# Performance work log

Measured on AMD Instinct MI355X. Metric: run time of the kernel, lower is better.

The kernel has to match this reference:

```python
import jax, jax.numpy as jnp
import numpy as np

B, S, IN, H = 64, 512, 256, 256
NH, E = 8, 5
DH = H // NH


def _ln(x, g, b, eps=1e-5):
    m = jnp.mean(x, -1, keepdims=True)
    v = jnp.mean((x - m) ** 2, -1, keepdims=True)
    return (x - m) / jnp.sqrt(v + eps) * g + b


def setup_inputs() -> dict:
    key = jax.random.key(0)
    ks = jax.random.split(key, 32)
    def p(i, shape, scale=0.05):
        return jax.random.normal(ks[i], shape, dtype=jnp.float32) * scale
    return {
        "x": jax.random.normal(ks[0], (B, S, IN), dtype=jnp.float32),
        "lengths": jax.random.randint(ks[1], (B,), 1, S + 1),
        "fe_w": p(2, (H, IN)), "fe_b": p(3, (H,)),
        "fe_ln_g": jnp.ones((H,), jnp.float32), "fe_ln_b": jnp.zeros((H,), jnp.float32),
        "w_ih": p(4, (4 * H, H)), "w_hh": p(5, (4 * H, H)),
        "b_ih": p(6, (4 * H,)), "b_hh": p(7, (4 * H,)),
        "attn_w": p(8, (3 * H, H)), "attn_b": p(9, (3 * H,)),
        "attn_ow": p(10, (H, H)), "attn_ob": p(11, (H,)),
        "ln1_g": jnp.ones((H,), jnp.float32), "ln1_b": jnp.zeros((H,), jnp.float32),
        "router_w": p(12, (H, E)),
        "e_w1": p(13, (E, H, H)), "e_b1": p(14, (E, H)),
        "e_w2": p(15, (E, H, H)), "e_b2": p(16, (E, H)),
        "ln2_g": jnp.ones((H,), jnp.float32), "ln2_b": jnp.zeros((H,), jnp.float32),
        "cl_w1": p(17, (H, H)), "cl_b1": p(18, (H,)),
        "cl_ln_g": jnp.ones((H,), jnp.float32), "cl_ln_b": jnp.zeros((H,), jnp.float32),
        "cl_w2": p(19, (1, H)), "cl_b2": p(20, (1,)),
    }


def _forward(x, lengths, fe_w, fe_b, fe_ln_g, fe_ln_b, w_ih, w_hh, b_ih, b_hh,
             attn_w, attn_b, attn_ow, attn_ob, ln1_g, ln1_b, router_w,
             e_w1, e_b1, e_w2, e_b2, ln2_g, ln2_b,
             cl_w1, cl_b1, cl_ln_g, cl_ln_b, cl_w2, cl_b2):
    # feature extractor: Linear -> LayerNorm -> ReLU (dropout off at eval)
    h0 = jax.nn.relu(_ln(x @ fe_w.T + fe_b, fe_ln_g, fe_ln_b))  # [B,S,H]
    # single-layer LSTM over padded sequence (causal => matches packed outputs at t < len)
    def step(carry, xt):
        h, c = carry
        z = xt @ w_ih.T + b_ih + h @ w_hh.T + b_hh  # PyTorch gate order i,f,g,o
        i, f, g, o = jnp.split(z, 4, axis=-1)
        c = jax.nn.sigmoid(f) * c + jax.nn.sigmoid(i) * jnp.tanh(g)
        h = jax.nn.sigmoid(o) * jnp.tanh(c)
        return (h, c), h
    init = (jnp.zeros((B, H), x.dtype), jnp.zeros((B, H), x.dtype))
    _, outs = jax.lax.scan(step, init, jnp.swapaxes(h0, 0, 1))
    lstm_out = jnp.swapaxes(outs, 0, 1)  # [B,S,H]
    valid = jnp.arange(S)[None, :] < lengths[:, None]  # [B,S]
    lstm_out = lstm_out * valid[..., None]  # pad_packed_sequence zeros
    # multi-head self-attention with key padding mask
    qkv = lstm_out @ attn_w.T + attn_b
    q, k, v = jnp.split(qkv, 3, axis=-1)
    q = q.reshape(B, S, NH, DH)
    k = k.reshape(B, S, NH, DH)
    v = v.reshape(B, S, NH, DH)
    scores = jnp.einsum("bqhd,bkhd->bhqk", q, k) / jnp.sqrt(jnp.float32(DH))
    scores = jnp.where(valid[:, None, None, :], scores, jnp.float32(-1e9))
    attn = jax.nn.softmax(scores, axis=-1)
    ao = jnp.einsum("bhqk,bkhd->bqhd", attn, v).reshape(B, S, H)
    ao = ao @ attn_ow.T + attn_ob
    src = _ln(lstm_out + ao, ln1_g, ln1_b)  # post-norm residual
    # Switch (top-1) MoE FFN
    probs = jax.nn.softmax(src @ router_w, axis=-1)  # [B,S,E]
    idx = jnp.argmax(probs, axis=-1)                 # [B,S]
    gate = jnp.take_along_axis(probs, idx[..., None], axis=-1)  # [B,S,1]
    eh = jax.nn.relu(jnp.einsum("bsd,edh->bseh", src, e_w1) + e_b1)
    ey = jnp.einsum("bseh,ehd->bsed", eh, e_w2) + e_b2          # [B,S,E,H]
    ysel = jnp.take_along_axis(ey, idx[:, :, None, None], axis=2)[:, :, 0, :]
    out = _ln(src + gate * ysel, ln2_g, ln2_b)
    # masked mean pool
    out = out * valid[..., None]
    pooled = out.sum(axis=1) / lengths[:, None].astype(jnp.float32)
    # classifier head
    hcl = jax.nn.relu(_ln(pooled @ cl_w1.T + cl_b1, cl_ln_g, cl_ln_b))
    return hcl @ cl_w2.T + cl_b2  # [B,1]


def reference(x, lengths, fe_w, fe_b, fe_ln_g, fe_ln_b, w_ih, w_hh, b_ih, b_hh,
              attn_w, attn_b, attn_ow, attn_ob, ln1_g, ln1_b, router_w,
              e_w1, e_b1, e_w2, e_b2, ln2_g, ln2_b,
              cl_w1, cl_b1, cl_ln_g, cl_ln_b, cl_w2, cl_b2):
    return _forward(x, lengths, fe_w, fe_b, fe_ln_g, fe_ln_b, w_ih, w_hh, b_ih, b_hh,
                    attn_w, attn_b, attn_ow, attn_ob, ln1_g, ln1_b, router_w,
                    e_w1, e_b1, e_w2, e_b2, ln2_g, ln2_b,
                    cl_w1, cl_b1, cl_ln_g, cl_ln_b, cl_w2, cl_b2)
```

## Files before the change

kernel.cpp:

```cpp
#include <hip/hip_runtime.h>
#include <cstdio>
#include <math.h>

#define BB 64
#define SS 512
#define HH 256
#define G4 1024
#define TT (BB*SS)

typedef _Float16 h2 __attribute__((ext_vector_type(2)));
typedef _Float16 h8 __attribute__((ext_vector_type(8)));
typedef float f4v __attribute__((ext_vector_type(4)));

__device__ __forceinline__ float sigf(float x){ return 1.0f/(1.0f+expf(-x)); }

__global__ void prep_kernel(const float* __restrict__ b_ih, const float* __restrict__ b_hh,
                            float* __restrict__ bcomb, float* __restrict__ hglob,
                            unsigned* __restrict__ cnt){
    int i = blockIdx.x*blockDim.x + threadIdx.x;
    if (i < G4) bcomb[i] = b_ih[i] + b_hh[i];
    if (i < 8)  cnt[i] = 0u;
    hglob[i] = 0.f;
}

__global__ __launch_bounds__(256) void gemm_mfma(
    const float* __restrict__ A, const float* __restrict__ Bw,
    const float* __restrict__ bias, float* __restrict__ C,
    int N, const int* __restrict__ lengths)
{
    int m0 = blockIdx.y * 128, n0 = blockIdx.x * 128;
    if (lengths){ int b = m0 >> 9, t0 = m0 & 511; if (t0 >= lengths[b]) return; }
    __shared__ _Float16 Asd[128][40];
    __shared__ _Float16 Bsd[128][40];
    int tid = threadIdx.x;
    int wave = tid >> 6, lane = tid & 63;
    int wr = (wave >> 1) * 64, wc = (wave & 1) * 64;
    int fr = lane & 15, fk = (lane >> 4) * 8;
    int srow = tid >> 1, skh = (tid & 1) * 16;
    const float* gA = A  + (size_t)(m0 + srow)*256 + skh;
    const float* gB = Bw + (size_t)(n0 + srow)*256 + skh;
    f4v acc[4][4];
    #pragma unroll
    for (int i=0;i<4;i++)
        #pragma unroll
        for (int j=0;j<4;j++) acc[i][j] = (f4v){0.f,0.f,0.f,0.f};

    for (int kt = 0; kt < 8; ++kt){
        int k0 = kt*32;
        float4 a0 = *(const float4*)(gA + k0);
        float4 a1 = *(const float4*)(gA + k0 + 4);
        float4 a2 = *(const float4*)(gA + k0 + 8);
        float4 a3 = *(const float4*)(gA + k0 + 12);
        float4 b0 = *(const float4*)(gB + k0);
        float4 b1 = *(const float4*)(gB + k0 + 4);
        float4 b2 = *(const float4*)(gB + k0 + 8);
        float4 b3 = *(const float4*)(gB + k0 + 12);
        __syncthreads();
        {
            _Float16* da = &Asd[srow][skh];
            h2 t;
            t.x=(_Float16)a0.x; t.y=(_Float16)a0.y; *(h2*)(da+0)=t;
            t.x=(_Float16)a0.z; t.y=(_Float16)a0.w; *(h2*)(da+2)=t;
            t.x=(_Float16)a1.x; t.y=(_Float16)a1.y; *(h2*)(da+4)=t;
            t.x=(_Float16)a1.z; t.y=(_Float16)a1.w; *(h2*)(da+6)=t;
            t.x=(_Float16)a2.x; t.y=(_Float16)a2.y; *(h2*)(da+8)=t;
            t.x=(_Float16)a2.z; t.y=(_Float16)a2.w; *(h2*)(da+10)=t;
            t.x=(_Float16)a3.x; t.y=(_Float16)a3.y; *(h2*)(da+12)=t;
            t.x=(_Float16)a3.z; t.y=(_Float16)a3.w; *(h2*)(da+14)=t;
            _Float16* db = &Bsd[srow][skh];
            t.x=(_Float16)b0.x; t.y=(_Float16)b0.y; *(h2*)(db+0)=t;
            t.x=(_Float16)b0.z; t.y=(_Float16)b0.w; *(h2*)(db+2)=t;
            t.x=(_Float16)b1.x; t.y=(_Float16)b1.y; *(h2*)(db+4)=t;
            t.x=(_Float16)b1.z; t.y=(_Float16)b1.w; *(h2*)(db+6)=t;
            t.x=(_Float16)b2.x; t.y=(_Float16)b2.y; *(h2*)(db+8)=t;
            t.x=(_Float16)b2.z; t.y=(_Float16)b2.w; *(h2*)(db+10)=t;
            t.x=(_Float16)b3.x; t.y=(_Float16)b3.y; *(h2*)(db+12)=t;
            t.x=(_Float16)b3.z; t.y=(_Float16)b3.w; *(h2*)(db+14)=t;
        }
        __syncthreads();
        h8 af[4], bf[4];
        #pragma unroll
        for (int mt=0;mt<4;mt++) af[mt] = *(const h8*)&Asd[wr + mt*16 + fr][fk];
        #pragma unroll
        for (int nt=0;nt<4;nt++) bf[nt] = *(const h8*)&Bsd[wc + nt*16 + fr][fk];
        #pragma unroll
        for (int mt=0;mt<4;mt++)
            #pragma unroll
            for (int nt=0;nt<4;nt++)
                acc[mt][nt] = __builtin_amdgcn_mfma_f32_16x16x32_f16(af[mt], bf[nt], acc[mt][nt], 0,0,0);
    }
    int rbase = m0 + wr + (lane>>4)*4;
    #pragma unroll
    for (int nt=0;nt<4;nt++){
        int col = n0 + wc + nt*16 + fr;
        float bv = bias ? bias[col] : 0.f;
        #pragma unroll
        for (int mt=0;mt<4;mt++){
            int row = rbase + mt*16;
            #pragma unroll
            for (int j=0;j<4;j++)
                C[(size_t)(row+j)*N + col] = acc[mt][nt][j] + bv;
        }
    }
}

__global__ __launch_bounds__(256) void ln_act(
    float* __restrict__ X, const float* __restrict__ add,
    const float* __restrict__ gg, const float* __restrict__ bb,
    const int* __restrict__ lengths, int relu)
{
    int row = blockIdx.x;
    { int b = row >> 9, t = row & 511; if (t >= lengths[b]) return; }
    int tid = threadIdx.x;
    __shared__ float red[8];
    size_t idx = (size_t)row*HH + tid;
    float v = X[idx];
    if (add) v += add[idx];
    float s = v, q = v*v;
    #pragma unroll
    for (int m=32;m>=1;m>>=1){ s += __shfl_xor(s,m); q += __shfl_xor(q,m); }
    if ((tid&63)==0){ red[tid>>6]=s; red[4+(tid>>6)]=q; }
    __syncthreads();
    s = red[0]+red[1]+red[2]+red[3]; q = red[4]+red[5]+red[6]+red[7];
    float mean = s*(1.f/HH);
    float var  = q*(1.f/HH) - mean*mean;
    float rstd = rsqrtf(var + 1e-5f);
    float o = (v-mean)*rstd*gg[tid] + bb[tid];
    if (relu) o = fmaxf(o, 0.f);
    X[idx] = o;
}

__global__ __launch_bounds__(512) void lstm_kernel(
    const float* __restrict__ Zx, const float* __restrict__ whh,
    const int* __restrict__ lengths, float* __restrict__ hglob,
    float* __restrict__ out)
{
    int bid = blockIdx.x;
    int row = bid >> 1, p = bid & 1;
    int tid = threadIdx.x;
    __shared__ __align__(16) _Float16 hs_own[128];
    __shared__ __align__(16) _Float16 hs_rem[128];
    __shared__ float zfull[512];

    int q = tid >> 7, d = tid & 127;
    const float* wrow = whh + (size_t)(q*256 + p*128 + d)*256;
    const float* wown = wrow + p*128;
    const float* wrem = wrow + (1-p)*128;
    h2 wA[64], wB[64];
    #pragma unroll
    for (int c=0;c<32;c++){
        float4 w4 = *(const float4*)(wown + c*4);
        h2 a; a.x=(_Float16)w4.x; a.y=(_Float16)w4.y;
        h2 b; b.x=(_Float16)w4.z; b.y=(_Float16)w4.w;
        wA[2*c]=a; wA[2*c+1]=b;
    }
    #pragma unroll
    for (int c=0;c<32;c++){
        float4 w4 = *(const float4*)(wrem + c*4);
        h2 a; a.x=(_Float16)w4.x; a.y=(_Float16)w4.y;
        h2 b; b.x=(_Float16)w4.z; b.y=(_Float16)w4.w;
        wB[2*c]=a; wB[2*c+1]=b;
    }
    int Tg = lengths[row];
    float creg = 0.f;

    if (tid < 64) ((unsigned*)hs_own)[tid] = 0u;
    else if (tid < 128) ((unsigned*)hs_rem)[tid-64] = 0u;
    __syncthreads();

    float zx0=0.f, zx1=0.f, zx2=0.f, zx3=0.f;
    size_t zbase = (size_t)row*SS*G4 + (size_t)(p*128 + tid);
    if (tid < 128 && Tg > 0){
        zx0 = Zx[zbase      ];
        zx1 = Zx[zbase + 256];
        zx2 = Zx[zbase + 512];
        zx3 = Zx[zbase + 768];
    }

    unsigned long long* hgl64 = (unsigned long long*)hglob;
    union U16 { float4 f; h2 h[4]; };

    for (int s = 0; s < Tg; ++s){
        bool pollme = (tid < 64) && (s > 0);
        unsigned tagP = ((unsigned)s & 7u) ^ 5u;
        size_t paddr = ((size_t)((s&1)*64 + row)*2 + (1-p))*64 + tid;
        unsigned long long pv = 0;
        if (pollme) pv = __hip_atomic_load(&hgl64[paddr], __ATOMIC_RELAXED, __HIP_MEMORY_SCOPE_AGENT);

        float accA = 0.f, accB = 0.f;
        #pragma unroll
        for (int c=0;c<16;c++){
            U16 u; u.f = *(const float4*)&hs_own[c*8];
            accA = __builtin_amdgcn_fdot2(u.h[0], wA[c*4+0], accA, false);
            accB = __builtin_amdgcn_fdot2(u.h[1], wA[c*4+1], accB, false);
            accA = __builtin_amdgcn_fdot2(u.h[2], wA[c*4+2], accA, false);
            accB = __builtin_amdgcn_fdot2(u.h[3], wA[c*4+3], accB, false);
        }
        if (pollme){
            while ((((unsigned)pv & 7u) != tagP) || (((unsigned)(pv>>32) & 7u) != tagP))
                pv = __hip_atomic_load(&hgl64[paddr], __ATOMIC_RELAXED, __HIP_MEMORY_SCOPE_AGENT);
            h2 t; t.x = (_Float16)__uint_as_float((unsigned)pv);
            t.y = (_Float16)__uint_as_float((unsigned)(pv>>32));
            ((h2*)hs_rem)[tid] = t;
        }
        asm volatile("s_waitcnt lgkmcnt(0)" ::: "memory");
        __builtin_amdgcn_s_barrier();
        asm volatile("" ::: "memory");

        #pragma unroll
        for (int c=0;c<16;c++){
            U16 u; u.f = *(const float4*)&hs_rem[c*8];
            accA = __builtin_amdgcn_fdot2(u.h[0], wB[c*4+0], accA, false);
            accB = __builtin_amdgcn_fdot2(u.h[1], wB[c*4+1], accB, false);
            accA = __builtin_amdgcn_fdot2(u.h[2], wB[c*4+2], accA, false);
            accB = __builtin_amdgcn_fdot2(u.h[3], wB[c*4+3], accB, false);
        }
        zfull[tid] = accA + accB;
        asm volatile("s_waitcnt lgkmcnt(0)" ::: "memory");
        __builtin_amdgcn_s_barrier();
        asm volatile("" ::: "memory");

        if (tid < 128){
            float z0 = zfull[tid      ] + zx0;
            float z1 = zfull[128 + tid] + zx1;
            float z2 = zfull[256 + tid] + zx2;
            float z3 = zfull[384 + tid] + zx3;
            if (s+1 < Tg){
                size_t zb = zbase + (size_t)(s+1)*G4;
                zx0 = Zx[zb      ];
                zx1 = Zx[zb + 256];
                zx2 = Zx[zb + 512];
                zx3 = Zx[zb + 768];
            }
            creg = sigf(z1)*creg + sigf(z0)*tanhf(z2);
            float hvv = sigf(z3)*tanhf(creg);
            int buf2 = (s+1) & 1;
            unsigned tag2 = (((unsigned)(s+1)) & 7u) ^ 5u;
            unsigned hb = (__float_as_uint(hvv) & ~7u) | tag2;
            float hm = __uint_as_float(hb);
            __hip_atomic_store(&hglob[((size_t)(buf2*64 + row)*2 + p)*128 + tid],
                               hm, __ATOMIC_RELAXED, __HIP_MEMORY_SCOPE_AGENT);
            out[((size_t)row*SS + s)*HH + p*128 + tid] = hvv;
            hs_own[tid] = (_Float16)hm;
        }
        asm volatile("s_waitcnt lgkmcnt(0)" ::: "memory");
        __builtin_amdgcn_s_barrier();
        asm volatile("" ::: "memory");
    }
}

__global__ __launch_bounds__(256) void attn_kernel(
    const float* __restrict__ qkv, const int* __restrict__ lengths, float* __restrict__ ctx)
{
    int bh = blockIdx.x; int b = bh >> 3, h = bh & 7;
    int len = lengths[b];
    int tid = threadIdx.x;
    __shared__ float Ks[512][32];
    __shared__ float Vs[512][32];
    for (int i = tid; i < len*32; i += 256){
        int s = i >> 5, d = i & 31;
        size_t base = ((size_t)b*512 + s)*768 + h*32 + d;
        Ks[s][d] = qkv[base + 256];
        Vs[s][d] = qkv[base + 512];
    }
    __syncthreads();
    const float rs = 0.1767766952966369f;
    for (int q0 = 0; q0 < 512; q0 += 256){
        int q = q0 + tid;
        if (q >= len) continue;
        float qr[32];
        size_t qb = ((size_t)b*512 + q)*768 + h*32;
        #pragma unroll
        for (int d=0; d<32; d+=4){
            float4 t4 = *(const float4*)&qkv[qb+d];
            qr[d]=t4.x; qr[d+1]=t4.y; qr[d+2]=t4.z; qr[d+3]=t4.w;
        }
        float m = -3.4e38f, l = 0.f, acc[32];
        #pragma unroll
        for (int d=0;d<32;d++) acc[d]=0.f;
        for (int k=0;k<len;k++){
            float sc = 0.f;
            #pragma unroll
            for (int d=0;d<32;d+=4){
                float4 kv = *(const float4*)&Ks[k][d];
                sc += qr[d]*kv.x + qr[d+1]*kv.y + qr[d+2]*kv.z + qr[d+3]*kv.w;
            }
            sc *= rs;
            float nm = fmaxf(m, sc);
            float f  = expf(m - nm);
            float pc = expf(sc - nm);
            l = l*f + pc;
            #pragma unroll
            for (int d=0;d<32;d+=4){
                float4 vv = *(const float4*)&Vs[k][d];
                acc[d]   = acc[d]*f   + pc*vv.x;
                acc[d+1] = acc[d+1]*f + pc*vv.y;
                acc[d+2] = acc[d+2]*f + pc*vv.z;
                acc[d+3] = acc[d+3]*f + pc*vv.w;
            }
            m = nm;
        }
        float inv = 1.f/l;
        size_t cb = ((size_t)b*512 + q)*256 + h*32;
        #pragma unroll
        for (int d=0;d<32;d+=4){
            float4 o; o.x=acc[d]*inv; o.y=acc[d+1]*inv; o.z=acc[d+2]*inv; o.w=acc[d+3]*inv;
            *(float4*)&ctx[cb+d] = o;
        }
    }
}

__global__ __launch_bounds__(256) void route_kernel(
    const float* __restrict__ src, const float* __restrict__ rw,
    const int* __restrict__ lengths, unsigned* __restrict__ cnt,
    int* __restrict__ bucket, float* __restrict__ gates)
{
    int wv = threadIdx.x >> 6, lane = threadIdx.x & 63;
    int tok = blockIdx.x*4 + wv;
    int b = tok >> 9, t = tok & 511;
    if (t >= lengths[b]) return;
    float4 xv = *(const float4*)&src[(size_t)tok*256 + lane*4];
    float l0,l1,l2,l3,l4;
    {
        const float* r0 = &rw[(lane*4)*5];
        l0 = xv.x*r0[0] + xv.y*r0[5] + xv.z*r0[10] + xv.w*r0[15];
        l1 = xv.x*r0[1] + xv.y*r0[6] + xv.z*r0[11] + xv.w*r0[16];
        l2 = xv.x*r0[2] + xv.y*r0[7] + xv.z*r0[12] + xv.w*r0[17];
        l3 = xv.x*r0[3] + xv.y*r0[8] + xv.z*r0[13] + xv.w*r0[18];
        l4 = xv.x*r0[4] + xv.y*r0[9] + xv.z*r0[14] + xv.w*r0[19];
    }
    #pragma unroll
    for (int m=32;m>=1;m>>=1){
        l0 += __shfl_xor(l0,m); l1 += __shfl_xor(l1,m); l2 += __shfl_xor(l2,m);
        l3 += __shfl_xor(l3,m); l4 += __shfl_xor(l4,m);
    }
    if (lane == 0){
        float mx = l0; int ix = 0;
        if (l1 > mx){ mx=l1; ix=1; }
        if (l2 > mx){ mx=l2; ix=2; }
        if (l3 > mx){ mx=l3; ix=3; }
        if (l4 > mx){ mx=l4; ix=4; }
        float ssum = expf(l0-mx)+expf(l1-mx)+expf(l2-mx)+expf(l3-mx)+expf(l4-mx);
        int slot = (int)atomicAdd(&cnt[ix], 1u);
        bucket[ix*32768 + slot] = tok;
        gates[tok] = 1.0f/ssum;
    }
}

__global__ __launch_bounds__(256) void moe_gemm(
    const float* __restrict__ src, const int* __restrict__ bucket,
    const unsigned* __restrict__ cnt, const float* __restrict__ gates,
    const float* __restrict__ w1, const float* __restrict__ b1,
    const float* __restrict__ w2, const float* __restrict__ b2,
    const float* __restrict__ g2, const float* __restrict__ bt2,
    float* __restrict__ out)
{
    int e = blockIdx.y;
    int count = (int)cnt[e];
    int start = blockIdx.x*64;
    if (start >= count) return;
    int n = min(64, count-start);
    __shared__ float sv[64][256];
    __shared__ float hv[64][256];
    __shared__ int   toks[64];
    __shared__ float gts[64];
    int tid = threadIdx.x;
    if (tid < 64){
        int idx = start + min(tid, n-1);
        int tk = bucket[e*32768 + idx];
        toks[tid] = tk;
        gts[tid]  = gates[tk];
    }
    __syncthreads();
    for (int i=0;i<64;i++)
        sv[i][tid] = src[(size_t)toks[i]*256 + tid];
    __syncthreads();
    int tt = tid >> 5, dd = tid & 31;
    const float* W1 = w1 + (size_t)e*65536;
    const float* W2 = w2 + (size_t)e*65536;
    float acc[8][8];
    {
        float4 bA = *(const float4*)&b1[e*256 + dd*8];
        float4 bB = *(const float4*)&b1[e*256 + dd*8 + 4];
        #pragma unroll
        for (int i=0;i<8;i++){
            acc[i][0]=bA.x; acc[i][1]=bA.y; acc[i][2]=bA.z; acc[i][3]=bA.w;
            acc[i][4]=bB.x; acc[i][5]=bB.y; acc[i][6]=bB.z; acc[i][7]=bB.w;
        }
    }
    #pragma unroll 2
    for (int k=0;k<256;k++){
        float4 wA = *(const float4*)&W1[(size_t)k*256 + dd*8];
        float4 wB = *(const float4*)&W1[(size_t)k*256 + dd*8 + 4];
        float wv0=wA.x,wv1=wA.y,wv2=wA.z,wv3=wA.w,wv4=wB.x,wv5=wB.y,wv6=wB.z,wv7=wB.w;
        #pragma unroll
        for (int i=0;i<8;i++){
            float hvv = sv[tt*8+i][k];
            acc[i][0]=fmaf(hvv,wv0,acc[i][0]); acc[i][1]=fmaf(hvv,wv1,acc[i][1]);
            acc[i][2]=fmaf(hvv,wv2,acc[i][2]); acc[i][3]=fmaf(hvv,wv3,acc[i][3]);
            acc[i][4]=fmaf(hvv,wv4,acc[i][4]); acc[i][5]=fmaf(hvv,wv5,acc[i][5]);
            acc[i][6]=fmaf(hvv,wv6,acc[i][6]); acc[i][7]=fmaf(hvv,wv7,acc[i][7]);
        }
    }
    #pragma unroll
    for (int i=0;i<8;i++){
        #pragma unroll
        for (int j=0;j<8;j++) hv[tt*8+i][dd*8+j] = fmaxf(acc[i][j], 0.f);
    }
    __syncthreads();
    {
        float4 bA = *(const float4*)&b2[e*256 + dd*8];
        float4 bB = *(const float4*)&b2[e*256 + dd*8 + 4];
        #pragma unroll
        for (int i=0;i<8;i++){
            acc[i][0]=bA.x; acc[i][1]=bA.y; acc[i][2]=bA.z; acc[i][3]=bA.w;
            acc[i][4]=bB.x; acc[i][5]=bB.y; acc[i][6]=bB.z; acc[i][7]=bB.w;
        }
    }
    #pragma unroll 2
    for (int k=0;k<256;k++){
        float4 wA = *(const float4*)&W2[(size_t)k*256 + dd*8];
        float4 wB = *(const float4*)&W2[(size_t)k*256 + dd*8 + 4];
        float wv0=wA.x,wv1=wA.y,wv2=wA.z,wv3=wA.w,wv4=wB.x,wv5=wB.y,wv6=wB.z,wv7=wB.w;
        #pragma unroll
        for (int i=0;i<8;i++){
            float hvv = hv[tt*8+i][k];
            acc[i][0]=fmaf(hvv,wv0,acc[i][0]); acc[i][1]=fmaf(hvv,wv1,acc[i][1]);
            acc[i][2]=fmaf(hvv,wv2,acc[i][2]); acc[i][3]=fmaf(hvv,wv3,acc[i][3]);
            acc[i][4]=fmaf(hvv,wv4,acc[i][4]); acc[i][5]=fmaf(hvv,wv5,acc[i][5]);
            acc[i][6]=fmaf(hvv,wv6,acc[i][6]); acc[i][7]=fmaf(hvv,wv7,acc[i][7]);
        }
    }
    float4 gA = *(const float4*)&g2[dd*8];
    float4 gB = *(const float4*)&g2[dd*8 + 4];
    float4 tA = *(const float4*)&bt2[dd*8];
    float4 tB = *(const float4*)&bt2[dd*8 + 4];
    float gv[8] = {gA.x,gA.y,gA.z,gA.w,gB.x,gB.y,gB.z,gB.w};
    float tv[8] = {tA.x,tA.y,tA.z,tA.w,tB.x,tB.y,tB.z,tB.w};
    #pragma unroll
    for (int i=0;i<8;i++){
        float gate = gts[tt*8+i];
        float4 sA = *(const float4*)&sv[tt*8+i][dd*8];
        float4 sB = *(const float4*)&sv[tt*8+i][dd*8 + 4];
        float svv[8] = {sA.x,sA.y,sA.z,sA.w,sB.x,sB.y,sB.z,sB.w};
        float s = 0.f, q = 0.f;
        #pragma unroll
        for (int j=0;j<8;j++){
            float r = svv[j] + gate*acc[i][j];
            acc[i][j] = r;
            s += r; q += r*r;
        }
        #pragma unroll
        for (int m=16;m>=1;m>>=1){ s += __shfl_xor(s,m); q += __shfl_xor(q,m); }
        float mean = s*(1.f/256.f), var = q*(1.f/256.f)-mean*mean;
        float rstd = rsqrtf(var + 1e-5f);
        if (tt*8+i < n){
            int tok = toks[tt*8+i];
            float o[8];
            #pragma unroll
            for (int j=0;j<8;j++) o[j] = (acc[i][j]-mean)*rstd*gv[j] + tv[j];
            float4 oA = make_float4(o[0],o[1],o[2],o[3]);
            float4 oB = make_float4(o[4],o[5],o[6],o[7]);
            *(float4*)&out[(size_t)tok*256 + dd*8]     = oA;
            *(float4*)&out[(size_t)tok*256 + dd*8 + 4] = oB;
        }
    }
}

__global__ __launch_bounds__(1024) void pool_kernel(
    const float* __restrict__ out2, const int* __restrict__ lengths, float* __restrict__ pooled)
{
    int b = blockIdx.x;
    int d = threadIdx.x & 255, c = threadIdx.x >> 8;
    int len = lengths[b];
    __shared__ float part[4][256];
    float s = 0.f;
    for (int t=c; t<len; t+=4) s += out2[((size_t)b*512+t)*256 + d];
    part[c][d] = s;
    __syncthreads();
    if (c==0) pooled[b*256+d] = (part[0][d]+part[1][d]+part[2][d]+part[3][d]) / (float)len;
}

__global__ __launch_bounds__(256) void cls_kernel(
    const float* __restrict__ pooled, const float* __restrict__ w1,
    const float* __restrict__ b1, const float* __restrict__ lg, const float* __restrict__ lb,
    const float* __restrict__ w2, const float* __restrict__ b2, float* __restrict__ outp)
{
    int b = blockIdx.x, j = threadIdx.x;
    __shared__ float pv[256];
    __shared__ float red[8];
    pv[j] = pooled[b*256 + j];
    __syncthreads();
    float acc = b1[j];
    for (int d=0; d<256; d+=4){
        float4 p4 = *(const float4*)&pv[d];
        const float* wr = &w1[(size_t)j*256 + d];
        acc += p4.x*wr[0] + p4.y*wr[1] + p4.z*wr[2] + p4.w*wr[3];
    }
    float s = acc, q = acc*acc;
    #pragma unroll
    for (int m=32;m>=1;m>>=1){ s += __shfl_xor(s,m); q += __shfl_xor(q,m); }
    int wid = j>>6;
    if ((j&63)==0){ red[wid]=s; red[4+wid]=q; }
    __syncthreads();
    s = red[0]+red[1]+red[2]+red[3]; q = red[4]+red[5]+red[6]+red[7];
    float mean = s*(1.f/256.f), var = q*(1.f/256.f)-mean*mean, rstd = rsqrtf(var+1e-5f);
    float h1v = fmaxf((acc-mean)*rstd*lg[j]+lb[j], 0.f);
    float pr = h1v * w2[j];
    __syncthreads();
    #pragma unroll
    for (int m=32;m>=1;m>>=1) pr += __shfl_xor(pr,m);
    if ((j&63)==0) red[wid] = pr;
    __syncthreads();
    if (j==0) outp[b] = red[0]+red[1]+red[2]+red[3] + b2[0];
}

extern "C" void kernel_launch(void* const* d_in, const int* in_sizes, int n_in,
                              void* d_out, int out_size, void* d_ws, size_t ws_size,
                              hipStream_t stream)
{
    const float* x       = (const float*)d_in[0];
    const int*   lengths = (const int*)  d_in[1];
    const float* fe_w    = (const float*)d_in[2];
    const float* fe_b    = (const float*)d_in[3];
    const float* fe_ln_g = (const float*)d_in[4];
    const float* fe_ln_b = (const float*)d_in[5];
    const float* w_ih    = (const float*)d_in[6];
    const float* w_hh    = (const float*)d_in[7];
    const float* b_ih    = (const float*)d_in[8];
    const float* b_hh    = (const float*)d_in[9];
    const float* attn_w  = (const float*)d_in[10];
    const float* attn_b  = (const float*)d_in[11];
    const float* attn_ow = (const float*)d_in[12];
    const float* attn_ob = (const float*)d_in[13];
    const float* ln1_g   = (const float*)d_in[14];
    const float* ln1_b   = (const float*)d_in[15];
    const float* router_w= (const float*)d_in[16];
    const float* e_w1    = (const float*)d_in[17];
    const float* e_b1    = (const float*)d_in[18];
    const float* e_w2    = (const float*)d_in[19];
    const float* e_b2    = (const float*)d_in[20];
    const float* ln2_g   = (const float*)d_in[21];
    const float* ln2_b   = (const float*)d_in[22];
    const float* cl_w1   = (const float*)d_in[23];
    const float* cl_b1   = (const float*)d_in[24];
    const float* cl_ln_g = (const float*)d_in[25];
    const float* cl_ln_b = (const float*)d_in[26];
    const float* cl_w2   = (const float*)d_in[27];
    const float* cl_b2   = (const float*)d_in[28];
    float* outp = (float*)d_out;

    const size_t NEED = (size_t)50381832 * 4;
    if (ws_size < NEED){
        fprintf(stderr, "kernel_launch: ws too small (%zu < %zu)\n", ws_size, NEED);
        return;
    }
    float* W     = (float*)d_ws;
    float* h0    = W;
    float* Zx    = W + 8388608;
    float* lstm  = W + 41943040;
    float* hglob = W + 50331648;
    float* pooled= W + 50364416;
    float* bcomb = W + 50380800;
    float* qkv  = Zx;
    float* ctx  = Zx + 25165824;
    float* aop  = h0;
    float* src  = lstm;
    float* out2 = Zx;
    float*    gates  = h0;
    int*      bucket = (int*)(h0 + 32768);
    unsigned* cnt    = (unsigned*)pooled;

    prep_kernel<<<dim3(128), 256, 0, stream>>>(b_ih, b_hh, bcomb, hglob, cnt);
    gemm_mfma<<<dim3(2,256), 256, 0, stream>>>(x, fe_w, fe_b, h0, 256, lengths);
    ln_act<<<dim3(32768), 256, 0, stream>>>(h0, nullptr, fe_ln_g, fe_ln_b, lengths, 1);
    gemm_mfma<<<dim3(8,256), 256, 0, stream>>>(h0, w_ih, bcomb, Zx, 1024, lengths);
    lstm_kernel<<<dim3(128), 512, 0, stream>>>(Zx, w_hh, lengths, hglob, lstm);
    gemm_mfma<<<dim3(6,256), 256, 0, stream>>>(lstm, attn_w, attn_b, qkv, 768, lengths);
    attn_kernel<<<dim3(512), 256, 0, stream>>>(qkv, lengths, ctx);
    gemm_mfma<<<dim3(2,256), 256, 0, stream>>>(ctx, attn_ow, attn_ob, aop, 256, lengths);
    ln_act<<<dim3(32768), 256, 0, stream>>>(src, aop, ln1_g, ln1_b, lengths, 0);
    route_kernel<<<dim3(8192), 256, 0, stream>>>(src, router_w, lengths, cnt, bucket, gates);
    moe_gemm<<<dim3(512,5), 256, 0, stream>>>(src, bucket, cnt, gates,
                                              e_w1, e_b1, e_w2, e_b2, ln2_g, ln2_b, out2);
    pool_kernel<<<dim3(64), 1024, 0, stream>>>(out2, lengths, pooled);
    cls_kernel<<<dim3(64), 256, 0, stream>>>(pooled, cl_w1, cl_b1, cl_ln_g, cl_ln_b,
                                             cl_w2, cl_b2, outp);
}
```

Before: 2.018 ms.

## Use MFMA for LSTM recurrent matvec and flash-style attention

The LSTM recurrent step now computes the h·W_hh product with 16x16x32 f16 MFMA instructions, holding weight fragments in registers instead of using per-thread fdot2 loops. It also merges two barriers per step by having a spare wave poll the partner block's hidden state for the next step. The attention kernel is rewritten as an MFMA flash-attention loop with f16 K and transposed V in shared memory and online softmax done per 16-key tile. These changes target the ALU-bound recurrent loop and the scalar attention inner loop, at the cost of f16 precision in QK and PV and a riskier synchronisation ordering in the LSTM.

```diff
diff --git a/kernel.cpp b/kernel.cpp
--- a/kernel.cpp
+++ b/kernel.cpp
@@ -9,6 +9,7 @@
 #define TT (BB*SS)
 
 typedef _Float16 h2 __attribute__((ext_vector_type(2)));
+typedef _Float16 h4 __attribute__((ext_vector_type(4)));
 typedef _Float16 h8 __attribute__((ext_vector_type(8)));
 typedef float f4v __attribute__((ext_vector_type(4)));
 
@@ -138,34 +139,32 @@
     int bid = blockIdx.x;
     int row = bid >> 1, p = bid & 1;
     int tid = threadIdx.x;
-    __shared__ __align__(16) _Float16 hs_own[128];
-    __shared__ __align__(16) _Float16 hs_rem[128];
-    __shared__ float zfull[512];
-
-    int q = tid >> 7, d = tid & 127;
-    const float* wrow = whh + (size_t)(q*256 + p*128 + d)*256;
-    const float* wown = wrow + p*128;
-    const float* wrem = wrow + (1-p)*128;
-    h2 wA[64], wB[64];
-    #pragma unroll
-    for (int c=0;c<32;c++){
-        float4 w4 = *(const float4*)(wown + c*4);
-        h2 a; a.x=(_Float16)w4.x; a.y=(_Float16)w4.y;
-        h2 b; b.x=(_Float16)w4.z; b.y=(_Float16)w4.w;
-        wA[2*c]=a; wA[2*c+1]=b;
-    }
-    #pragma unroll
-    for (int c=0;c<32;c++){
-        float4 w4 = *(const float4*)(wrem + c*4);
-        h2 a; a.x=(_Float16)w4.x; a.y=(_Float16)w4.y;
-        h2 b; b.x=(_Float16)w4.z; b.y=(_Float16)w4.w;
-        wB[2*c]=a; wB[2*c+1]=b;
+    int wv = tid >> 6, lane = tid & 63;
+    int lr = lane & 15, lg = lane >> 4;
+    __shared__ __align__(16) _Float16 hs[256];
+    __shared__ __align__(16) float zfull[512];
+
+    h8 wfrag[4][8];
+    #pragma unroll
+    for (int i=0;i<4;i++){
+        int c = (wv*4+i)*16 + lr;
+        int q = c >> 7, dd = c & 127;
+        const float* wr_ = whh + (size_t)(q*256 + p*128 + dd)*256;
+        #pragma unroll
+        for (int kt=0;kt<8;kt++){
+            const float* src = wr_ + kt*32 + lg*8;
+            float4 w0 = *(const float4*)(src);
+            float4 w1 = *(const float4*)(src+4);
+            h8 f;
+            f[0]=(_Float16)w0.x; f[1]=(_Float16)w0.y; f[2]=(_Float16)w0.z; f[3]=(_Float16)w0.w;
+            f[4]=(_Float16)w1.x; f[5]=(_Float16)w1.y; f[6]=(_Float16)w1.z; f[7]=(_Float16)w1.w;
+            wfrag[i][kt] = f;
+        }
     }
     int Tg = lengths[row];
     float creg = 0.f;
 
-    if (tid < 64) ((unsigned*)hs_own)[tid] = 0u;
-    else if (tid < 128) ((unsigned*)hs_rem)[tid-64] = 0u;
+    if (tid < 128) ((unsigned*)hs)[tid] = 0u;
     __syncthreads();
 
     float zx0=0.f, zx1=0.f, zx2=0.f, zx3=0.f;
@@ -176,50 +175,33 @@
         zx2 = Zx[zbase + 512];
         zx3 = Zx[zbase + 768];
     }
-
     unsigned long long* hgl64 = (unsigned long long*)hglob;
-    union U16 { float4 f; h2 h[4]; };
+    int pt = tid - 256;
 
     for (int s = 0; s < Tg; ++s){
-        bool pollme = (tid < 64) && (s > 0);
-        unsigned tagP = ((unsigned)s & 7u) ^ 5u;
-        size_t paddr = ((size_t)((s&1)*64 + row)*2 + (1-p))*64 + tid;
-        unsigned long long pv = 0;
-        if (pollme) pv = __hip_atomic_load(&hgl64[paddr], __ATOMIC_RELAXED, __HIP_MEMORY_SCOPE_AGENT);
-
-        float accA = 0.f, accB = 0.f;
-        #pragma unroll
-        for (int c=0;c<16;c++){
-            U16 u; u.f = *(const float4*)&hs_own[c*8];
-            accA = __builtin_amdgcn_fdot2(u.h[0], wA[c*4+0], accA, false);
-            accB = __builtin_amdgcn_fdot2(u.h[1], wA[c*4+1], accB, false);
-            accA = __builtin_amdgcn_fdot2(u.h[2], wA[c*4+2], accA, false);
-            accB = __builtin_amdgcn_fdot2(u.h[3], wA[c*4+3], accB, false);
-        }
-        if (pollme){
-            while ((((unsigned)pv & 7u) != tagP) || (((unsigned)(pv>>32) & 7u) != tagP))
-                pv = __hip_atomic_load(&hgl64[paddr], __ATOMIC_RELAXED, __HIP_MEMORY_SCOPE_AGENT);
-            h2 t; t.x = (_Float16)__uint_as_float((unsigned)pv);
-            t.y = (_Float16)__uint_as_float((unsigned)(pv>>32));
-            ((h2*)hs_rem)[tid] = t;
-        }
         asm volatile("s_waitcnt lgkmcnt(0)" ::: "memory");
         __builtin_amdgcn_s_barrier();
         asm volatile("" ::: "memory");
 
-        #pragma unroll
-        for (int c=0;c<16;c++){
-            U16 u; u.f = *(const float4*)&hs_rem[c*8];
-            accA = __builtin_amdgcn_fdot2(u.h[0], wB[c*4+0], accA, false);
-            accB = __builtin_amdgcn_fdot2(u.h[1], wB[c*4+1], accB, false);
-            accA = __builtin_amdgcn_fdot2(u.h[2], wB[c*4+2], accA, false);
-            accB = __builtin_amdgcn_fdot2(u.h[3], wB[c*4+3], accB, false);
-        }
-        zfull[tid] = accA + accB;
+        h8 hfrag[8];
+        #pragma unroll
+        for (int kt=0;kt<8;kt++)
+            hfrag[kt] = *(const h8*)&hs[kt*32 + lg*8];
+        #pragma unroll
+        for (int i=0;i<4;i++){
+            f4v zacc = (f4v){0.f,0.f,0.f,0.f};
+            #pragma unroll
+            for (int kt=0;kt<8;kt++)
+                zacc = __builtin_amdgcn_mfma_f32_16x16x32_f16(wfrag[i][kt], hfrag[kt], zacc, 0,0,0);
+            if (lr == 0)
+                *(f4v*)&zfull[(wv*4+i)*16 + lg*4] = zacc;
+        }
         asm volatile("s_waitcnt lgkmcnt(0)" ::: "memory");
         __builtin_amdgcn_s_barrier();
         asm volatile("" ::: "memory");
 
+        int buf2 = (s+1) & 1;
+        unsigned tag2 = (((unsigned)(s+1)) & 7u) ^ 5u;
         if (tid < 128){
             float z0 = zfull[tid      ] + zx0;
             float z1 = zfull[128 + tid] + zx1;
@@ -234,18 +216,21 @@
             }
             creg = sigf(z1)*creg + sigf(z0)*tanhf(z2);
             float hvv = sigf(z3)*tanhf(creg);
-            int buf2 = (s+1) & 1;
-            unsigned tag2 = (((unsigned)(s+1)) & 7u) ^ 5u;
             unsigned hb = (__float_as_uint(hvv) & ~7u) | tag2;
             float hm = __uint_as_float(hb);
             __hip_atomic_store(&hglob[((size_t)(buf2*64 + row)*2 + p)*128 + tid],
                                hm, __ATOMIC_RELAXED, __HIP_MEMORY_SCOPE_AGENT);
             out[((size_t)row*SS + s)*HH + p*128 + tid] = hvv;
-            hs_own[tid] = (_Float16)hm;
-        }
-        asm volatile("s_waitcnt lgkmcnt(0)" ::: "memory");
-        __builtin_amdgcn_s_barrier();
-        asm volatile("" ::: "memory");
+            hs[p*128 + tid] = (_Float16)hm;
+        } else if (wv == 4 && (s+1) < Tg){
+            size_t paddr = ((size_t)(buf2*64 + row)*2 + (1-p))*64 + pt;
+            unsigned long long pv = __hip_atomic_load(&hgl64[paddr], __ATOMIC_RELAXED, __HIP_MEMORY_SCOPE_AGENT);
+            while ((((unsigned)pv & 7u) != tag2) || (((unsigned)(pv>>32) & 7u) != tag2))
+                pv = __hip_atomic_load(&hgl64[paddr], __ATOMIC_RELAXED, __HIP_MEMORY_SCOPE_AGENT);
+            h2 t; t.x = (_Float16)__uint_as_float((unsigned)pv);
+            t.y = (_Float16)__uint_as_float((unsigned)(pv>>32));
+            ((h2*)hs)[(1-p)*64 + pt] = t;
+        }
     }
 }
 
@@ -255,57 +240,100 @@
     int bh = blockIdx.x; int b = bh >> 3, h = bh & 7;
     int len = lengths[b];
     int tid = threadIdx.x;
-    __shared__ float Ks[512][32];
-    __shared__ float Vs[512][32];
-    for (int i = tid; i < len*32; i += 256){
-        int s = i >> 5, d = i & 31;
-        size_t base = ((size_t)b*512 + s)*768 + h*32 + d;
-        Ks[s][d] = qkv[base + 256];
-        Vs[s][d] = qkv[base + 512];
-    }
-    __syncthreads();
-    const float rs = 0.1767766952966369f;
-    for (int q0 = 0; q0 < 512; q0 += 256){
-        int q = q0 + tid;
-        if (q >= len) continue;
-        float qr[32];
-        size_t qb = ((size_t)b*512 + q)*768 + h*32;
-        #pragma unroll
-        for (int d=0; d<32; d+=4){
-            float4 t4 = *(const float4*)&qkv[qb+d];
-            qr[d]=t4.x; qr[d+1]=t4.y; qr[d+2]=t4.z; qr[d+3]=t4.w;
-        }
-        float m = -3.4e38f, l = 0.f, acc[32];
-        #pragma unroll
-        for (int d=0;d<32;d++) acc[d]=0.f;
-        for (int k=0;k<len;k++){
-            float sc = 0.f;
-            #pragma unroll
-            for (int d=0;d<32;d+=4){
-                float4 kv = *(const float4*)&Ks[k][d];
-                sc += qr[d]*kv.x + qr[d+1]*kv.y + qr[d+2]*kv.z + qr[d+3]*kv.w;
-            }
-            sc *= rs;
-            float nm = fmaxf(m, sc);
-            float f  = expf(m - nm);
-            float pc = expf(sc - nm);
-            l = l*f + pc;
-            #pragma unroll
-            for (int d=0;d<32;d+=4){
-                float4 vv = *(const float4*)&Vs[k][d];
-                acc[d]   = acc[d]*f   + pc*vv.x;
-                acc[d+1] = acc[d+1]*f + pc*vv.y;
-                acc[d+2] = acc[d+2]*f + pc*vv.z;
-                acc[d+3] = acc[d+3]*f + pc*vv.w;
-            }
-            m = nm;
-        }
-        float inv = 1.f/l;
+    int wv = tid >> 6, lane = tid & 63;
+    int lr = lane & 15, lg = lane >> 4;
+    __shared__ _Float16 Ks[512][32];
+    __shared__ _Float16 Vt[32][512];
+
+    #pragma unroll
+    for (int j = 0; j < 16; ++j){
+        int c = tid + j*256;
+        int key = c >> 3, d4 = (c & 7) * 4;
+        size_t base = ((size_t)b*512 + key)*768 + h*32 + d4;
+        float4 kv = *(const float4*)&qkv[base + 256];
+        float4 vvv = *(const float4*)&qkv[base + 512];
+        h2 k0; k0.x=(_Float16)kv.x; k0.y=(_Float16)kv.y;
+        h2 k1; k1.x=(_Float16)kv.z; k1.y=(_Float16)kv.w;
+        *(h2*)&Ks[key][d4]   = k0;
+        *(h2*)&Ks[key][d4+2] = k1;
+        Vt[d4+0][key] = (_Float16)vvv.x;
+        Vt[d4+1][key] = (_Float16)vvv.y;
+        Vt[d4+2][key] = (_Float16)vvv.z;
+        Vt[d4+3][key] = (_Float16)vvv.w;
+    }
+    __syncthreads();
+
+    h8 qf[8];
+    #pragma unroll
+    for (int i=0;i<8;i++){
+        int qt = wv + 4*i;
+        int q = qt*16 + lr;
+        size_t qb = ((size_t)b*512 + q)*768 + h*32 + lg*8;
+        float4 q0 = *(const float4*)&qkv[qb];
+        float4 q1 = *(const float4*)&qkv[qb+4];
+        h8 f;
+        f[0]=(_Float16)q0.x; f[1]=(_Float16)q0.y; f[2]=(_Float16)q0.z; f[3]=(_Float16)q0.w;
+        f[4]=(_Float16)q1.x; f[5]=(_Float16)q1.y; f[6]=(_Float16)q1.z; f[7]=(_Float16)q1.w;
+        qf[i] = f;
+    }
+    f4v oacc[8][2];
+    float mrow[8], lrow[8];
+    #pragma unroll
+    for (int i=0;i<8;i++){
+        oacc[i][0]=(f4v){0.f,0.f,0.f,0.f}; oacc[i][1]=(f4v){0.f,0.f,0.f,0.f};
+        mrow[i] = -3.0e38f; lrow[i] = 0.f;
+    }
+    const float sc = 0.1767766952966369f;
+    int ktmax = (len + 15) >> 4;
+    for (int kt = 0; kt < ktmax; ++kt){
+        h8 kf = *(const h8*)&Ks[kt*16 + lr][lg*8];
+        int keybase = kt*16 + lg*4;
+        h4 vf0, vf1;
+        #pragma unroll
+        for (int j=0;j<4;j++){
+            vf0[j] = Vt[lr][keybase + j];
+            vf1[j] = Vt[16+lr][keybase + j];
+        }
+        #pragma unroll
+        for (int i=0;i<8;i++){
+            int qt = wv + 4*i;
+            if (qt*16 >= len) continue;
+            f4v s4 = __builtin_amdgcn_mfma_f32_16x16x32_f16(kf, qf[i], (f4v){0.f,0.f,0.f,0.f}, 0,0,0);
+            float s0 = s4[0]*sc, s1 = s4[1]*sc, s2 = s4[2]*sc, s3 = s4[3]*sc;
+            if (keybase+0 >= len) s0 = -3.0e38f;
+            if (keybase+1 >= len) s1 = -3.0e38f;
+            if (keybase+2 >= len) s2 = -3.0e38f;
+            if (keybase+3 >= len) s3 = -3.0e38f;
+            float mt = fmaxf(fmaxf(s0,s1), fmaxf(s2,s3));
+            mt = fmaxf(mt, __shfl_xor(mt, 16));
+            mt = fmaxf(mt, __shfl_xor(mt, 32));
+            float mnew = fmaxf(mrow[i], mt);
+            float scale = __expf(mrow[i] - mnew);
+            float p0 = __expf(s0 - mnew), p1 = __expf(s1 - mnew);
+            float p2 = __expf(s2 - mnew), p3 = __expf(s3 - mnew);
+            float psum = p0+p1+p2+p3;
+            psum += __shfl_xor(psum, 16);
+            psum += __shfl_xor(psum, 32);
+            lrow[i] = lrow[i]*scale + psum;
+            mrow[i] = mnew;
+            oacc[i][0] = oacc[i][0] * scale;
+            oacc[i][1] = oacc[i][1] * scale;
+            h4 pf; pf[0]=(_Float16)p0; pf[1]=(_Float16)p1; pf[2]=(_Float16)p2; pf[3]=(_Float16)p3;
+            oacc[i][0] = __builtin_amdgcn_mfma_f32_16x16x16f16(vf0, pf, oacc[i][0], 0,0,0);
+            oacc[i][1] = __builtin_amdgcn_mfma_f32_16x16x16f16(vf1, pf, oacc[i][1], 0,0,0);
+        }
+    }
+    #pragma unroll
+    for (int i=0;i<8;i++){
+        int qt = wv + 4*i;
+        if (qt*16 >= len) continue;
+        int q = qt*16 + lr;
+        float inv = 1.0f / lrow[i];
         size_t cb = ((size_t)b*512 + q)*256 + h*32;
         #pragma unroll
-        for (int d=0;d<32;d+=4){
-            float4 o; o.x=acc[d]*inv; o.y=acc[d+1]*inv; o.z=acc[d+2]*inv; o.w=acc[d+3]*inv;
-            *(float4*)&ctx[cb+d] = o;
+        for (int j=0;j<4;j++){
+            ctx[cb + lg*4 + j]      = oacc[i][0][j]*inv;
+            ctx[cb + 16 + lg*4 + j] = oacc[i][1][j]*inv;
         }
     }
 }
```

Result: faster. 1.770 ms (-12.3%).
